# Performance work log

Hardware: AMD Instinct MI355X
Metric: run time of the kernel (lower is better)

Reference implementation:

```python
import jax, jax.numpy as jnp
import numpy as np

MARGIN = 1.0
EPS = 1e-05
B = 8192
D = 128
NUM_CLASSES = 256


def setup_inputs() -> dict:
    key = jax.random.key(0)
    k1, k2 = jax.random.split(key)
    feature = jax.random.normal(k1, (B, D), dtype=jnp.float32)
    label = jax.random.randint(k2, (B,), 0, NUM_CLASSES, dtype=jnp.int32)
    return {"feature": feature, "label": label}


def reference(feature, label):
    # Pairwise Euclidean distance matrix: ||x_i||^2 + ||x_j||^2 - 2 x_i.x_j + eps, then sqrt
    sq = jnp.sum(feature * feature, axis=1, keepdims=True)  # [B, 1]
    dist = jnp.sqrt(jnp.maximum(sq + sq.T - 2.0 * (feature @ feature.T) + EPS, 0.0))  # [B, B]

    same = label[:, None] == label[None, :]  # [B, B] bool, includes self on diagonal
    inf = jnp.array(jnp.inf, dtype=dist.dtype)

    # Original sorts each row and takes same[1]: the SECOND smallest same-label distance
    # (the smallest is the anchor itself, distance sqrt(eps)).
    d_same = jnp.where(same, dist, inf)
    two_smallest = -jax.lax.top_k(-d_same, 2)[0]  # [B, 2], ascending smallest two
    pos = two_smallest[:, 1]  # nearest positive excluding self

    # diff.min(): hardest (closest) negative per row
    neg = jnp.min(jnp.where(same, inf, dist), axis=1)

    hinge = jnp.maximum(MARGIN + pos - neg, 0.0)
    return jnp.mean(hinge)
```

## Files before the change

kernel.cpp:

```cpp
#include <hip/hip_runtime.h>
#include <math.h>


#define BN 8192
#define MARGIN_F 1.0f
#define EPS_F 1e-5f
#define CLS_CAP 256

typedef __attribute__((ext_vector_type(8))) short short8;
typedef __attribute__((ext_vector_type(4))) float floatx4;

__device__ __forceinline__ unsigned short bf16_rne(float x, float& r) {
    unsigned u = __float_as_uint(x);
    u += 0x7FFF + ((u >> 16) & 1);
    unsigned short h = (unsigned short)(u >> 16);
    r = __uint_as_float(((unsigned)h) << 16);
    return h;
}

__global__ __launch_bounds__(256) void prep_kernel(const float* __restrict__ f,
                                                   const int* __restrict__ lbl,
                                                   short8* __restrict__ fbT,
                                                   float* __restrict__ sq,
                                                   int* __restrict__ cls_cnt,
                                                   int* __restrict__ cls_idx,
                                                   float* __restrict__ g_acc,
                                                   unsigned* __restrict__ counter) {
    int gid = blockIdx.x * 256 + threadIdx.x;
    if (gid == 0) { *g_acc = 0.f; *counter = 0u; }
    int row = gid >> 2, part = gid & 3;
    const float4* f4 = (const float4*)f + (size_t)row * 32 + part * 8;
    float s = 0.f;
#pragma unroll
    for (int cc = 0; cc < 4; ++cc) {
        float4 v0 = f4[cc * 2], v1 = f4[cc * 2 + 1];
        float r0, r1, r2, r3, r4, r5, r6, r7;
        short8 o;
        o[0] = (short)bf16_rne(v0.x, r0);
        o[1] = (short)bf16_rne(v0.y, r1);
        o[2] = (short)bf16_rne(v0.z, r2);
        o[3] = (short)bf16_rne(v0.w, r3);
        o[4] = (short)bf16_rne(v1.x, r4);
        o[5] = (short)bf16_rne(v1.y, r5);
        o[6] = (short)bf16_rne(v1.z, r6);
        o[7] = (short)bf16_rne(v1.w, r7);
        fbT[(size_t)(part * 4 + cc) * BN + row] = o;
        s += r0 * r0 + r1 * r1 + r2 * r2 + r3 * r3 +
             r4 * r4 + r5 * r5 + r6 * r6 + r7 * r7;
    }
    s += __shfl_xor(s, 1, 4);
    s += __shfl_xor(s, 2, 4);
    if (part == 0) {
        sq[row] = s;
        int l = lbl[row];
        int idx = atomicAdd(&cls_cnt[l], 1);
        if (idx < CLS_CAP) cls_idx[l * CLS_CAP + idx] = row;
    }
}

__global__ __launch_bounds__(64) void pos_kernel(const short8* __restrict__ fbT,
                                                 const int* __restrict__ cls_cnt,
                                                 const int* __restrict__ cls_idx,
                                                 const float* __restrict__ sq,
                                                 float* __restrict__ pos_d2) {
    __shared__ int midx[CLS_CAP];
    const int cls = blockIdx.x;
    int n = cls_cnt[cls];
    if (n <= 0) return;
    if (n > CLS_CAP) n = CLS_CAP;
    const int lane = threadIdx.x;
    const int q = lane >> 4, c = lane & 15;

    for (int s = lane; s < CLS_CAP; s += 64) {
        int slot = (s < n) ? s : 0;
        midx[s] = cls_idx[cls * CLS_CAP + slot];
    }
    __syncthreads();

    const int nt = (n + 63) >> 6;
    for (int it = 0; it < nt; ++it) {
        short8 a[4][4];
#pragma unroll
        for (int mf = 0; mf < 4; ++mf) {
            int row = midx[it * 64 + mf * 16 + c];
#pragma unroll
            for (int ks = 0; ks < 4; ++ks)
                a[mf][ks] = fbT[(size_t)(ks * 4 + q) * BN + row];
        }
        float s1[4][4], s2[4][4];
#pragma unroll
        for (int mf = 0; mf < 4; ++mf)
#pragma unroll
            for (int rg = 0; rg < 4; ++rg) { s1[mf][rg] = INFINITY; s2[mf][rg] = INFINITY; }

        for (int jt = 0; jt < nt; ++jt) {
            short8 b[4][4];
            float sjv[4];
#pragma unroll
            for (int nf = 0; nf < 4; ++nf) {
                int jrow = midx[jt * 64 + nf * 16 + c];
#pragma unroll
                for (int ks = 0; ks < 4; ++ks)
                    b[ks][nf] = fbT[(size_t)(ks * 4 + q) * BN + jrow];
                sjv[nf] = sq[jrow];
            }
            floatx4 acc[4][4];
#pragma unroll
            for (int mf = 0; mf < 4; ++mf)
#pragma unroll
                for (int nf = 0; nf < 4; ++nf) acc[mf][nf] = (floatx4)0.f;
#pragma unroll
            for (int ks = 0; ks < 4; ++ks)
#pragma unroll
                for (int mf = 0; mf < 4; ++mf)
#pragma unroll
                    for (int nf = 0; nf < 4; ++nf)
                        acc[mf][nf] = __builtin_amdgcn_mfma_f32_16x16x32_bf16(
                            a[mf][ks], b[ks][nf], acc[mf][nf], 0, 0, 0);
#pragma unroll
            for (int nf = 0; nf < 4; ++nf) {
                int jslot = jt * 64 + nf * 16 + c;
                bool valid = (jslot < n);
#pragma unroll
                for (int mf = 0; mf < 4; ++mf)
#pragma unroll
                    for (int rg = 0; rg < 4; ++rg) {
                        float v = fmaf(-2.0f, acc[mf][nf][rg], sjv[nf]);
                        float vs = valid ? v : INFINITY;
                        s2[mf][rg] = fminf(s2[mf][rg], fmaxf(s1[mf][rg], vs));
                        s1[mf][rg] = fminf(s1[mf][rg], vs);
                    }
            }
        }
#pragma unroll
        for (int m = 1; m < 16; m <<= 1) {
#pragma unroll
            for (int mf = 0; mf < 4; ++mf)
#pragma unroll
                for (int rg = 0; rg < 4; ++rg) {
                    float o1 = __shfl_xor(s1[mf][rg], m, 16);
                    float o2 = __shfl_xor(s2[mf][rg], m, 16);
                    float lo = fminf(s1[mf][rg], o1);
                    float hi = fminf(fmaxf(s1[mf][rg], o1), fminf(s2[mf][rg], o2));
                    s1[mf][rg] = lo; s2[mf][rg] = hi;
                }
        }
        if (c == 0) {
#pragma unroll
            for (int mf = 0; mf < 4; ++mf)
#pragma unroll
                for (int rg = 0; rg < 4; ++rg) {
                    int slot = it * 64 + mf * 16 + q * 4 + rg;
                    if (slot < n) {
                        int row = midx[slot];
                        pos_d2[row] = sq[row] + s2[mf][rg];
                    }
                }
        }
    }
}

__global__ __launch_bounds__(256, 3) void main_kernel(const short8* __restrict__ fbT,
                                                      const int* __restrict__ lbl,
                                                      const float* __restrict__ sq,
                                                      float* __restrict__ part) {
    const int t = threadIdx.x;
    const int lane = t & 63;
    const int wv = t >> 6;
    const int q = lane >> 4, c = lane & 15;
    const int i0 = blockIdx.x * 256 + wv * 64;
    const int g = blockIdx.y;

    short8 a[4][4];
#pragma unroll
    for (int mf = 0; mf < 4; ++mf) {
        int row = i0 + mf * 16 + c;
#pragma unroll
        for (int ks = 0; ks < 4; ++ks)
            a[mf][ks] = fbT[(size_t)(ks * 4 + q) * BN + row];
    }
    int li[4][4];
#pragma unroll
    for (int mf = 0; mf < 4; ++mf)
#pragma unroll
        for (int rg = 0; rg < 4; ++rg)
            li[mf][rg] = lbl[i0 + mf * 16 + q * 4 + rg];

    float n1[4][4];
#pragma unroll
    for (int mf = 0; mf < 4; ++mf)
#pragma unroll
        for (int rg = 0; rg < 4; ++rg) n1[mf][rg] = INFINITY;

#pragma unroll
    for (int jt = 0; jt < 4; ++jt) {
        const int j0 = g * 256 + jt * 64;
#pragma unroll
        for (int nf = 0; nf < 4; ++nf) {
            const int jc = j0 + nf * 16 + c;
            short8 b0 = fbT[(size_t)(0 * 4 + q) * BN + jc];
            short8 b1 = fbT[(size_t)(1 * 4 + q) * BN + jc];
            short8 b2 = fbT[(size_t)(2 * 4 + q) * BN + jc];
            short8 b3 = fbT[(size_t)(3 * 4 + q) * BN + jc];
            int lj = lbl[jc];
            float sj = sq[jc];

            floatx4 acc[4];
#pragma unroll
            for (int mf = 0; mf < 4; ++mf) acc[mf] = (floatx4)0.f;
#pragma unroll
            for (int mf = 0; mf < 4; ++mf)
                acc[mf] = __builtin_amdgcn_mfma_f32_16x16x32_bf16(a[mf][0], b0, acc[mf], 0, 0, 0);
#pragma unroll
            for (int mf = 0; mf < 4; ++mf)
                acc[mf] = __builtin_amdgcn_mfma_f32_16x16x32_bf16(a[mf][1], b1, acc[mf], 0, 0, 0);
#pragma unroll
            for (int mf = 0; mf < 4; ++mf)
                acc[mf] = __builtin_amdgcn_mfma_f32_16x16x32_bf16(a[mf][2], b2, acc[mf], 0, 0, 0);
#pragma unroll
            for (int mf = 0; mf < 4; ++mf)
                acc[mf] = __builtin_amdgcn_mfma_f32_16x16x32_bf16(a[mf][3], b3, acc[mf], 0, 0, 0);

#pragma unroll
            for (int mf = 0; mf < 4; ++mf)
#pragma unroll
                for (int rg = 0; rg < 4; ++rg) {
                    float v = fmaf(-2.0f, acc[mf][rg], sj);
                    float vd = (li[mf][rg] == lj) ? INFINITY : v;
                    n1[mf][rg] = fminf(n1[mf][rg], vd);
                }
        }
    }

#pragma unroll
    for (int m = 1; m < 16; m <<= 1) {
#pragma unroll
        for (int mf = 0; mf < 4; ++mf)
#pragma unroll
            for (int rg = 0; rg < 4; ++rg)
                n1[mf][rg] = fminf(n1[mf][rg], __shfl_xor(n1[mf][rg], m, 16));
    }
    if (c == 0) {
#pragma unroll
        for (int mf = 0; mf < 4; ++mf)
#pragma unroll
            for (int rg = 0; rg < 4; ++rg)
                part[g * BN + i0 + mf * 16 + q * 4 + rg] = n1[mf][rg];
    }
}

__global__ __launch_bounds__(128) void merge_kernel(const float* __restrict__ part,
                                                    const float* __restrict__ sq,
                                                    const float* __restrict__ pos_d2,
                                                    float* __restrict__ g_acc,
                                                    unsigned* __restrict__ counter,
                                                    float* __restrict__ out) {
    int r = blockIdx.x * 128 + threadIdx.x;
    float n = INFINITY;
#pragma unroll
    for (int k = 0; k < 32; ++k) n = fminf(n, part[k * BN + r]);
    float si = sq[r];
    float pos = sqrtf(fmaxf(pos_d2[r] + EPS_F, 0.f));
    float neg = sqrtf(fmaxf(si + n + EPS_F, 0.f));
    float h = fmaxf(MARGIN_F + pos - neg, 0.f);
    __shared__ float red[2];
#pragma unroll
    for (int m = 32; m >= 1; m >>= 1) h += __shfl_down(h, m, 64);
    if ((threadIdx.x & 63) == 0) red[threadIdx.x >> 6] = h;
    __syncthreads();
    if (threadIdx.x == 0) {
        atomicAdd(g_acc, red[0] + red[1]);
        __threadfence();
        unsigned old = atomicAdd(counter, 1u);
        if (old == 63u) {
            float tot = atomicAdd(g_acc, 0.0f);
            out[0] = tot / (float)BN;
        }
    }
}

extern "C" void kernel_launch(void* const* d_in, const int* in_sizes, int n_in,
                              void* d_out, int out_size, void* d_ws, size_t ws_size,
                              hipStream_t stream) {
    const float* f = (const float*)d_in[0];
    const int* lbl = (const int*)d_in[1];
    char* ws = (char*)d_ws;
    float* sq = (float*)ws;
    short8* fbT = (short8*)(ws + 32768);
    float* part = (float*)(ws + 32768 + 2097152);
    float* pos_d2 = (float*)(ws + 32768 + 2097152 + 1048576);
    float* g_acc = (float*)(ws + 32768 + 2097152 + 1048576 + 32768);
    unsigned* counter = (unsigned*)(g_acc + 1);
    int* cls_cnt = (int*)(ws + 32768 + 2097152 + 1048576 + 32768 + 128);
    int* cls_idx = (int*)((char*)cls_cnt + 1024);
    float* out = (float*)d_out;

    hipMemsetAsync(cls_cnt, 0, 256 * sizeof(int), stream);
    prep_kernel<<<128, 256, 0, stream>>>(f, lbl, fbT, sq, cls_cnt, cls_idx, g_acc, counter);
    pos_kernel<<<256, 64, 0, stream>>>(fbT, cls_cnt, cls_idx, sq, pos_d2);
    main_kernel<<<dim3(32, 32), 256, 0, stream>>>(fbT, lbl, sq, part);
    merge_kernel<<<64, 128, 0, stream>>>(part, sq, pos_d2, g_acc, counter, out);
}
```

Baseline: 103.7 us.

## Fuse positive and negative passes into one kernel with per-class label scan

Merges the per-class positive-distance kernel and the main negative-min kernel into a single launch. The first 256 blocks each scan the labels to build their class member list in shared memory, replacing the global atomic class bucketing and the memset. The negative blocks now cover 512 columns each, halving the partial-result count, and software-prefetch the next B fragment. Launch overhead and one kernel boundary go away, at the cost of every class block scanning all labels and uneven block work.

```diff
diff --git a/kernel.cpp b/kernel.cpp
--- a/kernel.cpp
+++ b/kernel.cpp
@@ -5,7 +5,6 @@
 #define BN 8192
 #define MARGIN_F 1.0f
 #define EPS_F 1e-5f
-#define CLS_CAP 256
 
 typedef __attribute__((ext_vector_type(8))) short short8;
 typedef __attribute__((ext_vector_type(4))) float floatx4;
@@ -19,11 +18,8 @@
 }
 
 __global__ __launch_bounds__(256) void prep_kernel(const float* __restrict__ f,
-                                                   const int* __restrict__ lbl,
                                                    short8* __restrict__ fbT,
                                                    float* __restrict__ sq,
-                                                   int* __restrict__ cls_cnt,
-                                                   int* __restrict__ cls_idx,
                                                    float* __restrict__ g_acc,
                                                    unsigned* __restrict__ counter) {
     int gid = blockIdx.x * 256 + threadIdx.x;
@@ -50,126 +46,118 @@
     }
     s += __shfl_xor(s, 1, 4);
     s += __shfl_xor(s, 2, 4);
-    if (part == 0) {
-        sq[row] = s;
-        int l = lbl[row];
-        int idx = atomicAdd(&cls_cnt[l], 1);
-        if (idx < CLS_CAP) cls_idx[l * CLS_CAP + idx] = row;
-    }
-}
-
-__global__ __launch_bounds__(64) void pos_kernel(const short8* __restrict__ fbT,
-                                                 const int* __restrict__ cls_cnt,
-                                                 const int* __restrict__ cls_idx,
-                                                 const float* __restrict__ sq,
-                                                 float* __restrict__ pos_d2) {
-    __shared__ int midx[CLS_CAP];
-    const int cls = blockIdx.x;
-    int n = cls_cnt[cls];
-    if (n <= 0) return;
-    if (n > CLS_CAP) n = CLS_CAP;
-    const int lane = threadIdx.x;
+    if (part == 0) sq[row] = s;
+}
+
+__global__ __launch_bounds__(256, 3) void work_kernel(const short8* __restrict__ fbT,
+                                                      const int* __restrict__ lbl,
+                                                      const float* __restrict__ sq,
+                                                      float* __restrict__ part,
+                                                      float* __restrict__ pos_d2) {
+    const int t = threadIdx.x;
+    const int lane = t & 63;
+    const int wv = t >> 6;
     const int q = lane >> 4, c = lane & 15;
-
-    for (int s = lane; s < CLS_CAP; s += 64) {
-        int slot = (s < n) ? s : 0;
-        midx[s] = cls_idx[cls * CLS_CAP + slot];
-    }
-    __syncthreads();
-
-    const int nt = (n + 63) >> 6;
-    for (int it = 0; it < nt; ++it) {
-        short8 a[4][4];
-#pragma unroll
-        for (int mf = 0; mf < 4; ++mf) {
-            int row = midx[it * 64 + mf * 16 + c];
-#pragma unroll
-            for (int ks = 0; ks < 4; ++ks)
-                a[mf][ks] = fbT[(size_t)(ks * 4 + q) * BN + row];
-        }
-        float s1[4][4], s2[4][4];
-#pragma unroll
-        for (int mf = 0; mf < 4; ++mf)
-#pragma unroll
-            for (int rg = 0; rg < 4; ++rg) { s1[mf][rg] = INFINITY; s2[mf][rg] = INFINITY; }
-
-        for (int jt = 0; jt < nt; ++jt) {
-            short8 b[4][4];
-            float sjv[4];
-#pragma unroll
-            for (int nf = 0; nf < 4; ++nf) {
-                int jrow = midx[jt * 64 + nf * 16 + c];
+    const int bid = blockIdx.x;
+
+    if (bid < 256) {
+        __shared__ int midx[256];
+        __shared__ int cnt;
+        const int cls = bid;
+        if (t == 0) cnt = 0;
+        __syncthreads();
+        for (int r = t; r < BN; r += 256) {
+            if (lbl[r] == cls) {
+                int p = atomicAdd(&cnt, 1);
+                if (p < 256) midx[p] = r;
+            }
+        }
+        __syncthreads();
+        int n = cnt < 256 ? cnt : 256;
+        if (n == 0) return;
+        int m0 = midx[0];
+        if (t >= n) midx[t] = m0;
+        __syncthreads();
+        if (wv != 0) return;
+
+        const int nt = (n + 63) >> 6;
+        for (int ip = 0; ip < 2 * nt; ++ip) {
+            short8 a[2][4];
+#pragma unroll
+            for (int mf = 0; mf < 2; ++mf) {
+                int row = midx[ip * 32 + mf * 16 + c];
 #pragma unroll
                 for (int ks = 0; ks < 4; ++ks)
-                    b[ks][nf] = fbT[(size_t)(ks * 4 + q) * BN + jrow];
-                sjv[nf] = sq[jrow];
-            }
-            floatx4 acc[4][4];
-#pragma unroll
-            for (int mf = 0; mf < 4; ++mf)
-#pragma unroll
-                for (int nf = 0; nf < 4; ++nf) acc[mf][nf] = (floatx4)0.f;
-#pragma unroll
-            for (int ks = 0; ks < 4; ++ks)
-#pragma unroll
-                for (int mf = 0; mf < 4; ++mf)
-#pragma unroll
-                    for (int nf = 0; nf < 4; ++nf)
-                        acc[mf][nf] = __builtin_amdgcn_mfma_f32_16x16x32_bf16(
-                            a[mf][ks], b[ks][nf], acc[mf][nf], 0, 0, 0);
-#pragma unroll
-            for (int nf = 0; nf < 4; ++nf) {
-                int jslot = jt * 64 + nf * 16 + c;
+                    a[mf][ks] = fbT[(size_t)(ks * 4 + q) * BN + row];
+            }
+            float s1[2][4], s2[2][4];
+#pragma unroll
+            for (int mf = 0; mf < 2; ++mf)
+#pragma unroll
+                for (int rg = 0; rg < 4; ++rg) { s1[mf][rg] = INFINITY; s2[mf][rg] = INFINITY; }
+
+            for (int s = 0; s < 4 * nt; ++s) {
+                int jslot = s * 16 + c;
+                int jrow = midx[jslot];
+                short8 b[4];
+#pragma unroll
+                for (int ks = 0; ks < 4; ++ks)
+                    b[ks] = fbT[(size_t)(ks * 4 + q) * BN + jrow];
+                float sj = sq[jrow];
                 bool valid = (jslot < n);
-#pragma unroll
-                for (int mf = 0; mf < 4; ++mf)
+
+                floatx4 acc[2];
+#pragma unroll
+                for (int mf = 0; mf < 2; ++mf) acc[mf] = (floatx4)0.f;
+#pragma unroll
+                for (int ks = 0; ks < 4; ++ks)
+#pragma unroll
+                    for (int mf = 0; mf < 2; ++mf)
+                        acc[mf] = __builtin_amdgcn_mfma_f32_16x16x32_bf16(
+                            a[mf][ks], b[ks], acc[mf], 0, 0, 0);
+#pragma unroll
+                for (int mf = 0; mf < 2; ++mf)
 #pragma unroll
                     for (int rg = 0; rg < 4; ++rg) {
-                        float v = fmaf(-2.0f, acc[mf][nf][rg], sjv[nf]);
+                        float v = fmaf(-2.0f, acc[mf][rg], sj);
                         float vs = valid ? v : INFINITY;
                         s2[mf][rg] = fminf(s2[mf][rg], fmaxf(s1[mf][rg], vs));
                         s1[mf][rg] = fminf(s1[mf][rg], vs);
                     }
             }
-        }
-#pragma unroll
-        for (int m = 1; m < 16; m <<= 1) {
-#pragma unroll
-            for (int mf = 0; mf < 4; ++mf)
-#pragma unroll
-                for (int rg = 0; rg < 4; ++rg) {
-                    float o1 = __shfl_xor(s1[mf][rg], m, 16);
-                    float o2 = __shfl_xor(s2[mf][rg], m, 16);
-                    float lo = fminf(s1[mf][rg], o1);
-                    float hi = fminf(fmaxf(s1[mf][rg], o1), fminf(s2[mf][rg], o2));
-                    s1[mf][rg] = lo; s2[mf][rg] = hi;
-                }
-        }
-        if (c == 0) {
-#pragma unroll
-            for (int mf = 0; mf < 4; ++mf)
-#pragma unroll
-                for (int rg = 0; rg < 4; ++rg) {
-                    int slot = it * 64 + mf * 16 + q * 4 + rg;
-                    if (slot < n) {
-                        int row = midx[slot];
-                        pos_d2[row] = sq[row] + s2[mf][rg];
+#pragma unroll
+            for (int m = 1; m < 16; m <<= 1) {
+#pragma unroll
+                for (int mf = 0; mf < 2; ++mf)
+#pragma unroll
+                    for (int rg = 0; rg < 4; ++rg) {
+                        float o1 = __shfl_xor(s1[mf][rg], m, 16);
+                        float o2 = __shfl_xor(s2[mf][rg], m, 16);
+                        float lo = fminf(s1[mf][rg], o1);
+                        float hi = fminf(fmaxf(s1[mf][rg], o1), fminf(s2[mf][rg], o2));
+                        s1[mf][rg] = lo; s2[mf][rg] = hi;
                     }
-                }
-        }
-    }
-}
-
-__global__ __launch_bounds__(256, 3) void main_kernel(const short8* __restrict__ fbT,
-                                                      const int* __restrict__ lbl,
-                                                      const float* __restrict__ sq,
-                                                      float* __restrict__ part) {
-    const int t = threadIdx.x;
-    const int lane = t & 63;
-    const int wv = t >> 6;
-    const int q = lane >> 4, c = lane & 15;
-    const int i0 = blockIdx.x * 256 + wv * 64;
-    const int g = blockIdx.y;
+            }
+            if (c == 0) {
+#pragma unroll
+                for (int mf = 0; mf < 2; ++mf)
+#pragma unroll
+                    for (int rg = 0; rg < 4; ++rg) {
+                        int islot = ip * 32 + mf * 16 + q * 4 + rg;
+                        if (islot < n) {
+                            int row = midx[islot];
+                            pos_d2[row] = sq[row] + s2[mf][rg];
+                        }
+                    }
+            }
+        }
+        return;
+    }
+
+    const int mbid = bid - 256;
+    const int i0 = (mbid & 31) * 256 + wv * 64;
+    const int g = mbid >> 5;
+    const int jb = g * 512;
 
     short8 a[4][4];
 #pragma unroll
@@ -192,44 +180,53 @@
 #pragma unroll
         for (int rg = 0; rg < 4; ++rg) n1[mf][rg] = INFINITY;
 
-#pragma unroll
-    for (int jt = 0; jt < 4; ++jt) {
-        const int j0 = g * 256 + jt * 64;
-#pragma unroll
-        for (int nf = 0; nf < 4; ++nf) {
-            const int jc = j0 + nf * 16 + c;
-            short8 b0 = fbT[(size_t)(0 * 4 + q) * BN + jc];
-            short8 b1 = fbT[(size_t)(1 * 4 + q) * BN + jc];
-            short8 b2 = fbT[(size_t)(2 * 4 + q) * BN + jc];
-            short8 b3 = fbT[(size_t)(3 * 4 + q) * BN + jc];
-            int lj = lbl[jc];
-            float sj = sq[jc];
-
-            floatx4 acc[4];
-#pragma unroll
-            for (int mf = 0; mf < 4; ++mf) acc[mf] = (floatx4)0.f;
-#pragma unroll
-            for (int mf = 0; mf < 4; ++mf)
-                acc[mf] = __builtin_amdgcn_mfma_f32_16x16x32_bf16(a[mf][0], b0, acc[mf], 0, 0, 0);
-#pragma unroll
-            for (int mf = 0; mf < 4; ++mf)
-                acc[mf] = __builtin_amdgcn_mfma_f32_16x16x32_bf16(a[mf][1], b1, acc[mf], 0, 0, 0);
-#pragma unroll
-            for (int mf = 0; mf < 4; ++mf)
-                acc[mf] = __builtin_amdgcn_mfma_f32_16x16x32_bf16(a[mf][2], b2, acc[mf], 0, 0, 0);
-#pragma unroll
-            for (int mf = 0; mf < 4; ++mf)
-                acc[mf] = __builtin_amdgcn_mfma_f32_16x16x32_bf16(a[mf][3], b3, acc[mf], 0, 0, 0);
-
-#pragma unroll
-            for (int mf = 0; mf < 4; ++mf)
-#pragma unroll
-                for (int rg = 0; rg < 4; ++rg) {
-                    float v = fmaf(-2.0f, acc[mf][rg], sj);
-                    float vd = (li[mf][rg] == lj) ? INFINITY : v;
-                    n1[mf][rg] = fminf(n1[mf][rg], vd);
-                }
-        }
+    int jc = jb + c;
+    short8 bc0 = fbT[(size_t)(q)*BN + jc];
+    short8 bc1 = fbT[(size_t)(4 + q) * BN + jc];
+    short8 bc2 = fbT[(size_t)(8 + q) * BN + jc];
+    short8 bc3 = fbT[(size_t)(12 + q) * BN + jc];
+    int ljc = lbl[jc];
+    float sjc = sq[jc];
+
+#pragma unroll
+    for (int s = 0; s < 32; ++s) {
+        short8 bn0, bn1, bn2, bn3;
+        int ljn; float sjn;
+        if (s < 31) {
+            int jn = jb + (s + 1) * 16 + c;
+            bn0 = fbT[(size_t)(q)*BN + jn];
+            bn1 = fbT[(size_t)(4 + q) * BN + jn];
+            bn2 = fbT[(size_t)(8 + q) * BN + jn];
+            bn3 = fbT[(size_t)(12 + q) * BN + jn];
+            ljn = lbl[jn];
+            sjn = sq[jn];
+        }
+        floatx4 acc[4];
+#pragma unroll
+        for (int mf = 0; mf < 4; ++mf) acc[mf] = (floatx4)0.f;
+#pragma unroll
+        for (int mf = 0; mf < 4; ++mf)
+            acc[mf] = __builtin_amdgcn_mfma_f32_16x16x32_bf16(a[mf][0], bc0, acc[mf], 0, 0, 0);
+#pragma unroll
+        for (int mf = 0; mf < 4; ++mf)
+            acc[mf] = __builtin_amdgcn_mfma_f32_16x16x32_bf16(a[mf][1], bc1, acc[mf], 0, 0, 0);
+#pragma unroll
+        for (int mf = 0; mf < 4; ++mf)
+            acc[mf] = __builtin_amdgcn_mfma_f32_16x16x32_bf16(a[mf][2], bc2, acc[mf], 0, 0, 0);
+#pragma unroll
+        for (int mf = 0; mf < 4; ++mf)
+            acc[mf] = __builtin_amdgcn_mfma_f32_16x16x32_bf16(a[mf][3], bc3, acc[mf], 0, 0, 0);
+
+#pragma unroll
+        for (int mf = 0; mf < 4; ++mf)
+#pragma unroll
+            for (int rg = 0; rg < 4; ++rg) {
+                float v = fmaf(-2.0f, acc[mf][rg], sjc);
+                float vd = (li[mf][rg] == ljc) ? INFINITY : v;
+                n1[mf][rg] = fminf(n1[mf][rg], vd);
+            }
+        bc0 = bn0; bc1 = bn1; bc2 = bn2; bc3 = bn3;
+        ljc = ljn; sjc = sjn;
     }
 
 #pragma unroll
@@ -258,7 +255,7 @@
     int r = blockIdx.x * 128 + threadIdx.x;
     float n = INFINITY;
 #pragma unroll
-    for (int k = 0; k < 32; ++k) n = fminf(n, part[k * BN + r]);
+    for (int k = 0; k < 16; ++k) n = fminf(n, part[k * BN + r]);
     float si = sq[r];
     float pos = sqrtf(fmaxf(pos_d2[r] + EPS_F, 0.f));
     float neg = sqrtf(fmaxf(si + n + EPS_F, 0.f));
@@ -288,16 +285,12 @@
     float* sq = (float*)ws;
     short8* fbT = (short8*)(ws + 32768);
     float* part = (float*)(ws + 32768 + 2097152);
-    float* pos_d2 = (float*)(ws + 32768 + 2097152 + 1048576);
-    float* g_acc = (float*)(ws + 32768 + 2097152 + 1048576 + 32768);
+    float* pos_d2 = (float*)(ws + 32768 + 2097152 + 524288);
+    float* g_acc = (float*)(ws + 32768 + 2097152 + 524288 + 32768);
     unsigned* counter = (unsigned*)(g_acc + 1);
-    int* cls_cnt = (int*)(ws + 32768 + 2097152 + 1048576 + 32768 + 128);
-    int* cls_idx = (int*)((char*)cls_cnt + 1024);
     float* out = (float*)d_out;
 
-    hipMemsetAsync(cls_cnt, 0, 256 * sizeof(int), stream);
-    prep_kernel<<<128, 256, 0, stream>>>(f, lbl, fbT, sq, cls_cnt, cls_idx, g_acc, counter);
-    pos_kernel<<<256, 64, 0, stream>>>(fbT, cls_cnt, cls_idx, sq, pos_d2);
-    main_kernel<<<dim3(32, 32), 256, 0, stream>>>(fbT, lbl, sq, part);
+    prep_kernel<<<128, 256, 0, stream>>>(f, fbT, sq, g_acc, counter);
+    work_kernel<<<768, 256, 0, stream>>>(fbT, lbl, sq, part, pos_d2);
     merge_kernel<<<64, 128, 0, stream>>>(part, sq, pos_d2, g_acc, counter, out);
 }
```

Measured after the change: 158.1 us. +52.5%, slower.
